# Optimization experiments

Hardware: AMD Instinct MI355X
Metric: run time of the kernel (lower is better)

## Reference

```python
import jax, jax.numpy as jnp
import numpy as np

N_NODES = 10000
N_EDGES = 160000
MUL0 = 128   # multiplicity of 0e in node input/output
MUL1 = 64    # multiplicity of 1o in node input/output
FC_IN = 8    # radial basis size (edge_scalar_attr dim)
FC_H = 64    # fc_neurons = [64, 64]
NUM_NEIGHBORS = 16.0
ANGLE = np.pi / 8.0
MID0 = MUL0 + MUL1   # 192 scalars in irreps_mid (simplified)
MID1 = MUL0 + MUL1   # 192 vectors (1o) in irreps_mid


def _inv_sqrt(d):
    return 1.0 / np.sqrt(d)


def setup_inputs() -> dict:
    key = jax.random.key(0)
    ks = jax.random.split(key, 18)
    rn = lambda k, shape: jax.random.normal(k, shape, dtype=jnp.float32)
    inp = {
        'node_input': rn(ks[0], (N_NODES, MUL0 + 3 * MUL1)),
        'edge_attr': rn(ks[1], (N_EDGES, 4)),            # 1x0e + 1x1o spherical harmonics
        'edge_scalar_attr': rn(ks[2], (N_EDGES, FC_IN)),
        # first Linear: node_input -> (node_features || node_self_out)
        'Wa0': rn(ks[3], (MUL0, MUL0)),   # 0e -> 0e (message branch)
        'Wa1': rn(ks[4], (MUL1, MUL1)),   # 1o -> 1o (message branch)
        'Wb0': rn(ks[5], (MUL0, MUL0)),   # 0e -> 0e (self branch)
        'Wb1': rn(ks[6], (MUL1, MUL1)),   # 1o -> 1o (self branch)
        # radial MLP
        'M1': rn(ks[7], (FC_IN, FC_H)),
        'M2': rn(ks[8], (FC_H, FC_H)),
        # per-instruction TP weight generators: [FC_H, mul] ('uvu', v=1 squeezed)
        'Wtp0': rn(ks[9], (FC_H, MUL0)),   # 0e x 0e -> 0e
        'Wtp1': rn(ks[10], (FC_H, MUL0)),  # 0e x 1o -> 1o
        'Wtp2': rn(ks[11], (FC_H, MUL1)),  # 1o x 0e -> 1o
        'Wtp3': rn(ks[12], (FC_H, MUL1)),  # 1o x 1o -> 0e
        # output Linear: irreps_mid (192x0e + 192x1o) -> 128x0e + 64x1o
        'Wo0': rn(ks[13], (MID0, MUL0)),
        'Wo1': rn(ks[14], (MID1, MUL1)),
        'edge_src': jax.random.randint(ks[15], (N_EDGES,), 0, N_NODES),
        'edge_dst': jax.random.randint(ks[16], (N_EDGES,), 0, N_NODES),
    }
    return inp


def _forward(node_input, edge_attr, edge_scalar_attr,
             Wa0, Wa1, Wb0, Wb1, M1, M2,
             Wtp0, Wtp1, Wtp2, Wtp3, Wo0, Wo1,
             edge_src, edge_dst):
    n = node_input.shape[0]
    x0 = node_input[:, :MUL0]                         # [N,128] 0e
    x1 = node_input[:, MUL0:].reshape(n, MUL1, 3)     # [N,64,3] 1o

    # Linear(node_input.irreps + irreps_node_output): split into message / self
    feat0 = (x0 @ Wa0) * _inv_sqrt(MUL0)
    feat1 = jnp.einsum('nvi,vu->nui', x1, Wa1) * _inv_sqrt(MUL1)
    self0 = (x0 @ Wb0) * _inv_sqrt(MUL0)
    self1 = jnp.einsum('nvi,vu->nui', x1, Wb1) * _inv_sqrt(MUL1)

    # gather node features to edges
    e0 = feat0[edge_src]                              # [E,128]
    e1 = feat1[edge_src]                              # [E,64,3]
    y0 = edge_attr[:, 0:1]                            # [E,1] 0e
    y1 = edge_attr[:, 1:4]                            # [E,3] 1o

    # radial MLP -> per-edge per-path 'uvu' weights (path param / sqrt(fc_out))
    h = jax.nn.gelu(edge_scalar_attr @ M1 * _inv_sqrt(FC_IN))
    h = jax.nn.gelu(h @ M2 * _inv_sqrt(FC_H))
    w0 = h @ Wtp0 * _inv_sqrt(FC_H)                   # [E,128]
    w1 = h @ Wtp1 * _inv_sqrt(FC_H)                   # [E,128]
    w2 = h @ Wtp2 * _inv_sqrt(FC_H)                   # [E,64]
    w3 = h @ Wtp3 * _inv_sqrt(FC_H)                   # [E,64]

    # CG tensor product paths (component normalization: alpha = sqrt(dim_out))
    mid0a = w0 * e0 * y0                                        # 0e x 0e -> 0e [E,128]
    mid0b = w3 * jnp.einsum('eui,ei->eu', e1, y1) * _inv_sqrt(3.0)  # 1o.1o -> 0e [E,64]
    mid1a = w1[:, :, None] * e0[:, :, None] * y1[:, None, :]   # 0e x 1o -> 1o [E,128,3]
    mid1b = w2[:, :, None] * e1 * y0[:, :, None]                # 1o x 0e -> 1o [E,64,3]

    e_cnt = edge_attr.shape[0]
    edge_mid = jnp.concatenate(
        [mid0a, mid0b, mid1a.reshape(e_cnt, -1), mid1b.reshape(e_cnt, -1)], axis=1)  # [E,768]

    # scatter-add to destination nodes, divide by sqrt(num_neighbors)
    agg = jax.ops.segment_sum(edge_mid, edge_dst, num_segments=n) * _inv_sqrt(NUM_NEIGHBORS)

    z0 = agg[:, :MID0]                                          # [N,192] 0e
    z1 = jnp.concatenate(
        [agg[:, MID0:MID0 + 3 * MUL0].reshape(n, MUL0, 3),
         agg[:, MID0 + 3 * MUL0:].reshape(n, MUL1, 3)], axis=1)  # [N,192,3] 1o

    conv0 = (z0 @ Wo0) * _inv_sqrt(MID0)
    conv1 = jnp.einsum('nvi,vu->nui', z1, Wo1) * _inv_sqrt(MID1)

    c = np.cos(ANGLE).astype(np.float32)
    s = np.sin(ANGLE).astype(np.float32)
    out0 = c * self0 + s * conv0                                 # [N,128]
    out1 = c * self1 + s * conv1                                 # [N,64,3]
    return jnp.concatenate([out0, out1.reshape(n, -1)], axis=1)  # [N,320]


def reference(node_input, edge_attr, edge_scalar_attr,
              Wa0, Wa1, Wb0, Wb1, M1, M2,
              Wtp0, Wtp1, Wtp2, Wtp3, Wo0, Wo1,
              edge_src, edge_dst):
    return _forward(node_input, edge_attr, edge_scalar_attr,
                    Wa0, Wa1, Wb0, Wb1, M1, M2,
                    Wtp0, Wtp1, Wtp2, Wtp3, Wo0, Wo1,
                    edge_src, edge_dst)
```

## Files before the change

### kernel.cpp

```cpp
#include <hip/hip_runtime.h>
#include <hip/hip_bf16.h>
#include <hip/hip_fp16.h>

#define N_NODES 10000
#define N_EDGES 160000
#define FEAT_W 320
#define CHUNK 32

typedef _Float16 half8 __attribute__((ext_vector_type(8)));
typedef float f32x4 __attribute__((ext_vector_type(4)));

__device__ __forceinline__ float gelu_tanh(float x) {
    float x3 = x * x * x;
    float y = 0.7978845608028654f * (x + 0.044715f * x3);
    float th = 1.f - 2.f / (__expf(2.f * y) + 1.f);
    return 0.5f * x * (1.f + th);
}

__global__ __launch_bounds__(320) void prep_kernel(
    const float* __restrict__ node_input,
    const float* __restrict__ Wa0, const float* __restrict__ Wa1,
    const float* __restrict__ Wb0, const float* __restrict__ Wb1,
    float* __restrict__ feat_tbl, float* __restrict__ self_tbl,
    const int* __restrict__ edge_dst, int* __restrict__ counts,
    int* __restrict__ rank,
    const float* __restrict__ Wtp0, const float* __restrict__ Wtp1,
    const float* __restrict__ Wtp2, const float* __restrict__ Wtp3,
    const float* __restrict__ Wo0,  const float* __restrict__ Wo1,
    __half* __restrict__ wtp_pack, __half* __restrict__ wo_pack)
{
    __shared__ __align__(16) float xT[FEAT_W][8];
    const int t = threadIdx.x;

    if (blockIdx.x < 1250) {
        const int node0 = blockIdx.x * 8;
        for (int q = t; q < 640; q += 320) {
            const int n = q / 80, c4 = q - n * 80;
            const float4 v = ((const float4*)(node_input + (size_t)(node0 + n) * FEAT_W))[c4];
            xT[c4 * 4 + 0][n] = v.x; xT[c4 * 4 + 1][n] = v.y;
            xT[c4 * 4 + 2][n] = v.z; xT[c4 * 4 + 3][n] = v.w;
        }
        __syncthreads();

        float accf[8] = {0,0,0,0,0,0,0,0}, accs[8] = {0,0,0,0,0,0,0,0};
        float scale;
        if (t < 128) {
            for (int v = 0; v < 128; ++v) {
                const float wa = Wa0[v * 128 + t];
                const float wb = Wb0[v * 128 + t];
                const float4 xa = *(const float4*)&xT[v][0];
                const float4 xb = *(const float4*)&xT[v][4];
                accf[0] += xa.x * wa; accf[1] += xa.y * wa; accf[2] += xa.z * wa; accf[3] += xa.w * wa;
                accf[4] += xb.x * wa; accf[5] += xb.y * wa; accf[6] += xb.z * wa; accf[7] += xb.w * wa;
                accs[0] += xa.x * wb; accs[1] += xa.y * wb; accs[2] += xa.z * wb; accs[3] += xa.w * wb;
                accs[4] += xb.x * wb; accs[5] += xb.y * wb; accs[6] += xb.z * wb; accs[7] += xb.w * wb;
            }
            scale = 0.08838834764831845f;
        } else {
            const int r = t - 128, u = r / 3, i = r - 3 * u;
            for (int v = 0; v < 64; ++v) {
                const float wa = Wa1[v * 64 + u];
                const float wb = Wb1[v * 64 + u];
                const int row = 128 + v * 3 + i;
                const float4 xa = *(const float4*)&xT[row][0];
                const float4 xb = *(const float4*)&xT[row][4];
                accf[0] += xa.x * wa; accf[1] += xa.y * wa; accf[2] += xa.z * wa; accf[3] += xa.w * wa;
                accf[4] += xb.x * wa; accf[5] += xb.y * wa; accf[6] += xb.z * wa; accf[7] += xb.w * wa;
                accs[0] += xa.x * wb; accs[1] += xa.y * wb; accs[2] += xa.z * wb; accs[3] += xa.w * wb;
                accs[4] += xb.x * wb; accs[5] += xb.y * wb; accs[6] += xb.z * wb; accs[7] += xb.w * wb;
            }
            scale = 0.125f;
        }
#pragma unroll
        for (int n = 0; n < 8; ++n) {
            feat_tbl[(size_t)(node0 + n) * FEAT_W + t] = accf[n] * scale;
            self_tbl[(size_t)(node0 + n) * FEAT_W + t] = accs[n] * scale;
        }
    } else if (blockIdx.x < 1750) {
        const int e = (blockIdx.x - 1250) * 320 + t;
        rank[e] = atomicAdd(&counts[edge_dst[e]], 1);
    } else {
        const int gid = (blockIdx.x - 1750) * 320 + t;
        if (gid < 1536) {
            const int lane = gid & 63;
            const int tile = gid >> 6;
            const int quad = lane >> 4, n16 = lane & 15;
            const int col = tile * 16 + n16;
            const float* src; int stride;
            if (col < 128)      { src = Wtp0 + col;         stride = 128; }
            else if (col < 256) { src = Wtp1 + (col - 128); stride = 128; }
            else if (col < 320) { src = Wtp2 + (col - 256); stride = 64;  }
            else                { src = Wtp3 + (col - 320); stride = 64;  }
            __half* dst = wtp_pack + (size_t)gid * 16;
#pragma unroll
            for (int s = 0; s < 2; ++s)
#pragma unroll
                for (int j = 0; j < 8; ++j)
                    dst[s * 8 + j] = (__half)src[(s * 32 + quad * 8 + j) * stride];
        } else if (gid < 38400) {
            const int i = gid - 1536;
            if (i < 24576) wo_pack[i] = (__half)Wo0[i];
            else           wo_pack[i] = (__half)Wo1[i - 24576];
        }
    }
}

__global__ __launch_bounds__(1024) void scan_kernel(
    const int* __restrict__ counts, int* __restrict__ offsets)
{
    __shared__ int wsum[16];
    const int wid = threadIdx.x >> 6, lane = threadIdx.x & 63;
    int base = 0;
    for (int c = 0; c < 10; ++c) {
        const int i = c * 1024 + threadIdx.x;
        const int v = (i < N_NODES) ? counts[i] : 0;
        int x = v;
#pragma unroll
        for (int off = 1; off < 64; off <<= 1) {
            int y = __shfl_up(x, off, 64);
            if (lane >= off) x += y;
        }
        if (lane == 63) wsum[wid] = x;
        __syncthreads();
        if (threadIdx.x < 16) {
            int s = wsum[threadIdx.x];
#pragma unroll
            for (int off = 1; off < 16; off <<= 1) {
                int y = __shfl_up(s, off, 64);
                if ((int)threadIdx.x >= off) s += y;
            }
            wsum[threadIdx.x] = s;
        }
        __syncthreads();
        const int waveoff = (wid == 0) ? 0 : wsum[wid - 1];
        const int excl = base + waveoff + x - v;
        if (i < N_NODES) offsets[i] = excl;
        const int tot = wsum[15];
        __syncthreads();
        base += tot;
    }
    if (threadIdx.x == 0) offsets[N_NODES] = base;
}

__global__ __launch_bounds__(512) void mlp_kernel(
    const float* __restrict__ esa,
    const float* __restrict__ M1,
    const float* __restrict__ M2,
    const int* __restrict__ edge_dst,
    const int* __restrict__ rank,
    const int* __restrict__ offsets,
    const int* __restrict__ edge_src,
    const float* __restrict__ edge_attr,
    __half* __restrict__ h2csr,
    int* __restrict__ srcs_csr,
    float* __restrict__ y4csr)
{
    __shared__ __align__(16) float sh[8][64];
    const int wave = threadIdx.x >> 6;
    const int lane = threadIdx.x & 63;
    const int e = blockIdx.x * 8 + wave;

    const int pos = offsets[edge_dst[e]] + rank[e];
    if (lane == 0) {
        srcs_csr[pos] = edge_src[e];
        ((float4*)y4csr)[pos] = ((const float4*)edge_attr)[e];
    }

    const float4 e0 = ((const float4*)(esa + (size_t)e * 8))[0];
    const float4 e1 = ((const float4*)(esa + (size_t)e * 8))[1];
    float h = e0.x * M1[0 * 64 + lane] + e0.y * M1[1 * 64 + lane]
            + e0.z * M1[2 * 64 + lane] + e0.w * M1[3 * 64 + lane]
            + e1.x * M1[4 * 64 + lane] + e1.y * M1[5 * 64 + lane]
            + e1.z * M1[6 * 64 + lane] + e1.w * M1[7 * 64 + lane];
    h = gelu_tanh(h * 0.35355339059327373f);
    sh[wave][lane] = h;
    __syncthreads();

    float h2 = 0.f;
    const float4* shp = (const float4*)sh[wave];
#pragma unroll
    for (int q = 0; q < 16; ++q) {
        const float4 s = shp[q];
        h2 += s.x * M2[(4 * q + 0) * 64 + lane];
        h2 += s.y * M2[(4 * q + 1) * 64 + lane];
        h2 += s.z * M2[(4 * q + 2) * 64 + lane];
        h2 += s.w * M2[(4 * q + 3) * 64 + lane];
    }
    h2 = gelu_tanh(h2 * 0.125f);
    h2csr[(size_t)pos * 64 + lane] = (__half)(h2 * 0.125f);
}

__global__ __launch_bounds__(384, 4) void gather_kernel(
    const int* __restrict__ offsets,
    const int* __restrict__ srcs_csr,
    const float* __restrict__ y4csr,
    const __half* __restrict__ h2csr,
    const __half* __restrict__ wtp_pack,
    const float* __restrict__ feat_tbl,
    const float* __restrict__ self_tbl,
    const __half* __restrict__ wo_pack,
    float* __restrict__ out)
{
    __shared__ __align__(16) __half wsh[CHUNK * 384];
    __shared__ __align__(16) char pool[CHUNK * 128];
    __shared__ float ys[CHUNK][4];
    __shared__ int   srcs[CHUNK];
    __half* h2s = (__half*)pool;
    float*  z   = (float*)pool;

    const int node = blockIdx.x;
    const int t = threadIdx.x;
    const int wave = t >> 6, lane = t & 63;
    const int quad = lane >> 4, n16 = lane & 15;
    const int G = t / 192;
    const int r = t - G * 192;

    const int beg = offsets[node], end = offsets[node + 1];

    int cb = beg;
    int ne = min(CHUNK, end - cb);
    half8 hreg = {};
    int   sreg = 0;
    float4 yreg = {0.f, 0.f, 0.f, 0.f};
    if (t < ne * 8) hreg = ((const half8*)(h2csr + (size_t)cb * 64))[t];
    if (t < ne)     { sreg = srcs_csr[cb + t]; yreg = ((const float4*)y4csr)[cb + t]; }

    half8 bf[4][2];
#pragma unroll
    for (int c = 0; c < 4; ++c) {
        const __half* p = wtp_pack + (size_t)((wave * 4 + c) * 64 + lane) * 16;
        bf[c][0] = *(const half8*)p;
        bf[c][1] = *(const half8*)(p + 8);
    }

    const int f0 = (r < 128) ? r : 128 + 3 * (r - 128);

    float acc = 0.f, acc3a = 0.f, acc3b = 0.f, acc3c = 0.f;

    for (;;) {
        if (t < ne) { srcs[t] = sreg; ((float4*)ys)[t] = yreg; }
        if (t < ne * 8) {
            const int eL = t >> 3, u = t & 7;
            *(half8*)((char*)h2s + eL * 128 + ((u * 16) ^ ((eL & 7) << 4))) = hreg;
        }
        __syncthreads();

#pragma unroll
        for (int g = 0; g < 2; ++g) {
            if (g * 16 < ne) {
                const int e = g * 16 + n16;
                const char* hb = (const char*)h2s + e * 128;
                const int sw = (e & 7) << 4;
                const half8 af0 = *(const half8*)(hb + ((quad * 16) ^ sw));
                const half8 af1 = *(const half8*)(hb + ((64 + quad * 16) ^ sw));
#pragma unroll
                for (int c = 0; c < 4; ++c) {
                    f32x4 acc4 = {0.f, 0.f, 0.f, 0.f};
                    acc4 = __builtin_amdgcn_mfma_f32_16x16x32_f16(af0, bf[c][0], acc4, 0, 0, 0);
                    acc4 = __builtin_amdgcn_mfma_f32_16x16x32_f16(af1, bf[c][1], acc4, 0, 0, 0);
                    const int colb = ((wave * 4 + c) * 16 + n16) * 2;
#pragma unroll
                    for (int rr = 0; rr < 4; ++rr) {
                        const int row = g * 16 + quad * 4 + rr;
                        *(__half*)((char*)wsh + row * 768 + (colb ^ (quad << 5))) =
                            (__half)acc4[rr];
                    }
                }
            }
        }

        const int cb2 = cb + CHUNK;
        const int ne2 = (cb2 < end) ? min(CHUNK, end - cb2) : 0;
        if (t < ne2 * 8) hreg = ((const half8*)(h2csr + (size_t)cb2 * 64))[t];
        if (t < ne2)     { sreg = srcs_csr[cb2 + t]; yreg = ((const float4*)y4csr)[cb2 + t]; }
        __syncthreads();

        const int h = (ne + 1) >> 1;
        const int eLo = G ? h : 0;
        const int eHi = G ? ne : h;
#define WRDC(ee, cc) __half2float(*(const __half*)((const char*)wsh + (ee) * 768 + (((cc) * 2) ^ ((((ee) >> 2) & 3) << 5))))
        if (r < 128) {
            int e = eLo;
            for (; e + 4 <= eHi; e += 4) {
                float wA[4], wB[4], v4[4]; int s4[4];
#pragma unroll
                for (int k = 0; k < 4; ++k) {
                    wA[k] = WRDC(e + k, r); wB[k] = WRDC(e + k, 128 + r);
                    s4[k] = srcs[e + k];
                }
#pragma unroll
                for (int k = 0; k < 4; ++k) v4[k] = feat_tbl[(size_t)s4[k] * FEAT_W + f0];
#pragma unroll
                for (int k = 0; k < 4; ++k) {
                    acc += wA[k] * v4[k] * ys[e + k][0];
                    const float p = wB[k] * v4[k];
                    acc3a += p * ys[e + k][1];
                    acc3b += p * ys[e + k][2];
                    acc3c += p * ys[e + k][3];
                }
            }
            for (; e < eHi; ++e) {
                const float v = feat_tbl[(size_t)srcs[e] * FEAT_W + f0];
                acc += WRDC(e, r) * v * ys[e][0];
                const float p = WRDC(e, 128 + r) * v;
                acc3a += p * ys[e][1]; acc3b += p * ys[e][2]; acc3c += p * ys[e][3];
            }
        } else {
            const int idx = r - 128;
            int e = eLo;
            for (; e + 4 <= eHi; e += 4) {
                float wC[4], wD[4], va[4], vb[4], vc[4]; int s4[4];
#pragma unroll
                for (int k = 0; k < 4; ++k) {
                    wC[k] = WRDC(e + k, 256 + idx); wD[k] = WRDC(e + k, 320 + idx);
                    s4[k] = srcs[e + k];
                }
#pragma unroll
                for (int k = 0; k < 4; ++k) {
                    const float* fr = feat_tbl + (size_t)s4[k] * FEAT_W;
                    va[k] = fr[f0]; vb[k] = fr[f0 + 1]; vc[k] = fr[f0 + 2];
                }
#pragma unroll
                for (int k = 0; k < 4; ++k) {
                    const float p = wC[k] * ys[e + k][0];
                    acc3a += p * va[k]; acc3b += p * vb[k]; acc3c += p * vc[k];
                    acc += wD[k] * (va[k] * ys[e + k][1] + vb[k] * ys[e + k][2]
                                  + vc[k] * ys[e + k][3]);
                }
            }
            for (; e < eHi; ++e) {
                const float* fr = feat_tbl + (size_t)srcs[e] * FEAT_W;
                const float va = fr[f0], vb = fr[f0 + 1], vc = fr[f0 + 2];
                const float p = WRDC(e, 256 + idx) * ys[e][0];
                acc3a += p * va; acc3b += p * vb; acc3c += p * vc;
                acc += WRDC(e, 320 + idx) * (va * ys[e][1] + vb * ys[e][2]
                                           + vc * ys[e][3]);
            }
        }
#undef WRDC

        if (!ne2) break;
        cb = cb2; ne = ne2;
        __syncthreads();
    }

    const float sZ = 0.25f;
    const float irt3 = 0.5773502691896258f;
    if (G == 0) {
        if (r < 128) {
            z[r]       = acc   * sZ;
            z[192 + r] = acc3a * sZ;
            z[384 + r] = acc3b * sZ;
            z[576 + r] = acc3c * sZ;
        } else {
            const int idx = r - 128;
            z[128 + idx] = acc * sZ * irt3;
            z[320 + idx] = acc3a * sZ;
            z[512 + idx] = acc3b * sZ;
            z[704 + idx] = acc3c * sZ;
        }
    }
    __syncthreads();
    if (G == 1) {
        if (r < 128) {
            z[r]       += acc   * sZ;
            z[192 + r] += acc3a * sZ;
            z[384 + r] += acc3b * sZ;
            z[576 + r] += acc3c * sZ;
        } else {
            const int idx = r - 128;
            z[128 + idx] += acc * sZ * irt3;
            z[320 + idx] += acc3a * sZ;
            z[512 + idx] += acc3b * sZ;
            z[704 + idx] += acc3c * sZ;
        }
    }
    __syncthreads();

    const float sA = 0.07216878364870323f;
    const float cR = 0.92387953251128674f;
    const float sR = 0.38268343236508978f;
    const __half* Wo0h = wo_pack;
    const __half* Wo1h = wo_pack + 24576;

    if (t < 128) {
        float conv = 0.f;
        const float4* z4 = (const float4*)z;
#pragma unroll 8
        for (int q = 0; q < 48; ++q) {
            const float4 zz = z4[q];
            conv += zz.x * (float)Wo0h[(4 * q + 0) * 128 + t];
            conv += zz.y * (float)Wo0h[(4 * q + 1) * 128 + t];
            conv += zz.z * (float)Wo0h[(4 * q + 2) * 128 + t];
            conv += zz.w * (float)Wo0h[(4 * q + 3) * 128 + t];
        }
        const float sv = self_tbl[(size_t)node * FEAT_W + t];
        out[(size_t)node * FEAT_W + t] = cR * sv + sR * conv * sA;
    } else if (t < 320) {
        const int idx = t - 128;
        const int i = idx >> 6, u = idx & 63;
        float conv = 0.f;
        const float4* z4 = (const float4*)(z + 192 + i * 192);
#pragma unroll 8
        for (int q = 0; q < 48; ++q) {
            const float4 zz = z4[q];
            conv += zz.x * (float)Wo1h[(4 * q + 0) * 64 + u];
            conv += zz.y * (float)Wo1h[(4 * q + 1) * 64 + u];
            conv += zz.z * (float)Wo1h[(4 * q + 2) * 64 + u];
            conv += zz.w * (float)Wo1h[(4 * q + 3) * 64 + u];
        }
        const int col = 128 + u * 3 + i;
        const float sv = self_tbl[(size_t)node * FEAT_W + col];
        out[(size_t)node * FEAT_W + col] = cR * sv + sR * conv * sA;
    }
}

extern "C" void kernel_launch(void* const* d_in, const int* in_sizes, int n_in,
                              void* d_out, int out_size, void* d_ws, size_t ws_size,
                              hipStream_t stream) {
    const float* node_input = (const float*)d_in[0];
    const float* edge_attr  = (const float*)d_in[1];
    const float* esa        = (const float*)d_in[2];
    const float* Wa0  = (const float*)d_in[3];
    const float* Wa1  = (const float*)d_in[4];
    const float* Wb0  = (const float*)d_in[5];
    const float* Wb1  = (const float*)d_in[6];
    const float* M1   = (const float*)d_in[7];
    const float* M2   = (const float*)d_in[8];
    const float* Wtp0 = (const float*)d_in[9];
    const float* Wtp1 = (const float*)d_in[10];
    const float* Wtp2 = (const float*)d_in[11];
    const float* Wtp3 = (const float*)d_in[12];
    const float* Wo0  = (const float*)d_in[13];
    const float* Wo1  = (const float*)d_in[14];
    const int* edge_src = (const int*)d_in[15];
    const int* edge_dst = (const int*)d_in[16];
    float* out = (float*)d_out;

    char* w = (char*)d_ws;
    float*  feat_tbl = (float*)w;           w += (size_t)N_NODES * FEAT_W * 4;
    float*  self_tbl = (float*)w;           w += (size_t)N_NODES * FEAT_W * 4;
    float*  y4csr    = (float*)w;           w += (size_t)N_EDGES * 4 * 4;
    __half* h2csr    = (__half*)w;          w += (size_t)N_EDGES * 64 * 2;
    __half* wtp_pack = (__half*)w;          w += (size_t)24576 * 2;
    __half* wo_pack  = (__half*)w;          w += (size_t)36864 * 2;
    int*    counts   = (int*)w;             w += (size_t)N_NODES * 4;
    int*    offsets  = (int*)w;             w += (size_t)(N_NODES + 1) * 4;
    int*    rank     = (int*)w;             w += (size_t)N_EDGES * 4;
    int*    srcs_csr = (int*)w;             w += (size_t)N_EDGES * 4;

    hipMemsetAsync(counts, 0, sizeof(int) * N_NODES, stream);

    prep_kernel<<<1870, 320, 0, stream>>>(node_input, Wa0, Wa1, Wb0, Wb1,
                                          feat_tbl, self_tbl,
                                          edge_dst, counts, rank,
                                          Wtp0, Wtp1, Wtp2, Wtp3, Wo0, Wo1,
                                          wtp_pack, wo_pack);
    scan_kernel<<<1, 1024, 0, stream>>>(counts, offsets);
    mlp_kernel<<<N_EDGES / 8, 512, 0, stream>>>(esa, M1, M2, edge_dst, rank, offsets,
                                                edge_src, edge_attr,
                                                h2csr, srcs_csr, y4csr);
    gather_kernel<<<N_NODES, 384, 0, stream>>>(offsets, srcs_csr, y4csr, h2csr,
                                               wtp_pack, feat_tbl, self_tbl,
                                               wo_pack, out);
}
```

Before: 408.7 us.

## Consume MFMA weight tiles directly in registers instead of staging through LDS

The per-edge tensor-product weights produced by MFMA are now used directly from the accumulator registers. Each wave multiplies them with gathered source features for its own column slice, accumulating per-lane partial sums that are reduced across quads with shuffles at the end. This removes the wsh LDS staging buffer, one barrier per chunk, and the two-group edge split. The cost is that each lane now issues more scattered feature gathers across its four edge rows and column groups, and the per-wave branch on irrep type may diverge.

```diff
diff --git a/kernel.cpp b/kernel.cpp
--- a/kernel.cpp
+++ b/kernel.cpp
@@ -201,7 +201,6 @@
     const __half* __restrict__ wo_pack,
     float* __restrict__ out)
 {
-    __shared__ __align__(16) __half wsh[CHUNK * 384];
     __shared__ __align__(16) char pool[CHUNK * 128];
     __shared__ float ys[CHUNK][4];
     __shared__ int   srcs[CHUNK];
@@ -212,8 +211,6 @@
     const int t = threadIdx.x;
     const int wave = t >> 6, lane = t & 63;
     const int quad = lane >> 4, n16 = lane & 15;
-    const int G = t / 192;
-    const int r = t - G * 192;
 
     const int beg = offsets[node], end = offsets[node + 1];
 
@@ -233,9 +230,7 @@
         bf[c][1] = *(const half8*)(p + 8);
     }
 
-    const int f0 = (r < 128) ? r : 128 + 3 * (r - 128);
-
-    float acc = 0.f, acc3a = 0.f, acc3b = 0.f, acc3c = 0.f;
+    float r0[4] = {0,0,0,0}, r1[4] = {0,0,0,0}, r2[4] = {0,0,0,0};
 
     for (;;) {
         if (t < ne) { srcs[t] = sreg; ((float4*)ys)[t] = yreg; }
@@ -245,134 +240,105 @@
         }
         __syncthreads();
 
-#pragma unroll
-        for (int g = 0; g < 2; ++g) {
-            if (g * 16 < ne) {
-                const int e = g * 16 + n16;
-                const char* hb = (const char*)h2s + e * 128;
-                const int sw = (e & 7) << 4;
-                const half8 af0 = *(const half8*)(hb + ((quad * 16) ^ sw));
-                const half8 af1 = *(const half8*)(hb + ((64 + quad * 16) ^ sw));
-#pragma unroll
-                for (int c = 0; c < 4; ++c) {
-                    f32x4 acc4 = {0.f, 0.f, 0.f, 0.f};
-                    acc4 = __builtin_amdgcn_mfma_f32_16x16x32_f16(af0, bf[c][0], acc4, 0, 0, 0);
-                    acc4 = __builtin_amdgcn_mfma_f32_16x16x32_f16(af1, bf[c][1], acc4, 0, 0, 0);
-                    const int colb = ((wave * 4 + c) * 16 + n16) * 2;
-#pragma unroll
-                    for (int rr = 0; rr < 4; ++rr) {
-                        const int row = g * 16 + quad * 4 + rr;
-                        *(__half*)((char*)wsh + row * 768 + (colb ^ (quad << 5))) =
-                            (__half)acc4[rr];
-                    }
-                }
-            }
-        }
-
         const int cb2 = cb + CHUNK;
         const int ne2 = (cb2 < end) ? min(CHUNK, end - cb2) : 0;
         if (t < ne2 * 8) hreg = ((const half8*)(h2csr + (size_t)cb2 * 64))[t];
         if (t < ne2)     { sreg = srcs_csr[cb2 + t]; yreg = ((const float4*)y4csr)[cb2 + t]; }
-        __syncthreads();
-
-        const int h = (ne + 1) >> 1;
-        const int eLo = G ? h : 0;
-        const int eHi = G ? ne : h;
-#define WRDC(ee, cc) __half2float(*(const __half*)((const char*)wsh + (ee) * 768 + (((cc) * 2) ^ ((((ee) >> 2) & 3) << 5))))
-        if (r < 128) {
-            int e = eLo;
-            for (; e + 4 <= eHi; e += 4) {
-                float wA[4], wB[4], v4[4]; int s4[4];
-#pragma unroll
-                for (int k = 0; k < 4; ++k) {
-                    wA[k] = WRDC(e + k, r); wB[k] = WRDC(e + k, 128 + r);
-                    s4[k] = srcs[e + k];
-                }
-#pragma unroll
-                for (int k = 0; k < 4; ++k) v4[k] = feat_tbl[(size_t)s4[k] * FEAT_W + f0];
-#pragma unroll
-                for (int k = 0; k < 4; ++k) {
-                    acc += wA[k] * v4[k] * ys[e + k][0];
-                    const float p = wB[k] * v4[k];
-                    acc3a += p * ys[e + k][1];
-                    acc3b += p * ys[e + k][2];
-                    acc3c += p * ys[e + k][3];
+
+#pragma unroll
+        for (int g = 0; g < 2; ++g) {
+            if (g * 16 < ne) {
+                const int er = g * 16 + n16;
+                const char* hb = (const char*)h2s + er * 128;
+                const int sw = (er & 7) << 4;
+                const half8 af0 = *(const half8*)(hb + ((quad * 16) ^ sw));
+                const half8 af1 = *(const half8*)(hb + ((64 + quad * 16) ^ sw));
+                f32x4 a0 = {0,0,0,0}, a1 = {0,0,0,0}, a2 = {0,0,0,0}, a3 = {0,0,0,0};
+                a0 = __builtin_amdgcn_mfma_f32_16x16x32_f16(af0, bf[0][0], a0, 0, 0, 0);
+                a0 = __builtin_amdgcn_mfma_f32_16x16x32_f16(af1, bf[0][1], a0, 0, 0, 0);
+                a1 = __builtin_amdgcn_mfma_f32_16x16x32_f16(af0, bf[1][0], a1, 0, 0, 0);
+                a1 = __builtin_amdgcn_mfma_f32_16x16x32_f16(af1, bf[1][1], a1, 0, 0, 0);
+                a2 = __builtin_amdgcn_mfma_f32_16x16x32_f16(af0, bf[2][0], a2, 0, 0, 0);
+                a2 = __builtin_amdgcn_mfma_f32_16x16x32_f16(af1, bf[2][1], a2, 0, 0, 0);
+                a3 = __builtin_amdgcn_mfma_f32_16x16x32_f16(af0, bf[3][0], a3, 0, 0, 0);
+                a3 = __builtin_amdgcn_mfma_f32_16x16x32_f16(af1, bf[3][1], a3, 0, 0, 0);
+
+#pragma unroll
+                for (int r = 0; r < 4; ++r) {
+                    const int e = g * 16 + quad * 4 + r;
+                    if (e < ne) {
+                        const float w4[4] = { a0[r], a1[r], a2[r], a3[r] };
+                        const float* fr = feat_tbl + (size_t)srcs[e] * FEAT_W;
+                        if (wave < 2) {
+                            const float y0 = ys[e][0];
+                            const int fb = wave * 64 + n16;
+#pragma unroll
+                            for (int c = 0; c < 4; ++c)
+                                r0[c] += w4[c] * fr[fb + c * 16] * y0;
+                        } else if (wave < 4) {
+                            const float y1 = ys[e][1], y2 = ys[e][2], y3 = ys[e][3];
+                            const int fb = (wave - 2) * 64 + n16;
+#pragma unroll
+                            for (int c = 0; c < 4; ++c) {
+                                const float p = w4[c] * fr[fb + c * 16];
+                                r0[c] += p * y1; r1[c] += p * y2; r2[c] += p * y3;
+                            }
+                        } else if (wave == 4) {
+                            const float y0 = ys[e][0];
+#pragma unroll
+                            for (int c = 0; c < 4; ++c) {
+                                const int f0 = 128 + 3 * (c * 16 + n16);
+                                const float p = w4[c] * y0;
+                                r0[c] += p * fr[f0];
+                                r1[c] += p * fr[f0 + 1];
+                                r2[c] += p * fr[f0 + 2];
+                            }
+                        } else {
+                            const float y1 = ys[e][1], y2 = ys[e][2], y3 = ys[e][3];
+#pragma unroll
+                            for (int c = 0; c < 4; ++c) {
+                                const int f0 = 128 + 3 * (c * 16 + n16);
+                                r0[c] += w4[c] * (fr[f0] * y1 + fr[f0 + 1] * y2
+                                                + fr[f0 + 2] * y3);
+                            }
+                        }
+                    }
                 }
             }
-            for (; e < eHi; ++e) {
-                const float v = feat_tbl[(size_t)srcs[e] * FEAT_W + f0];
-                acc += WRDC(e, r) * v * ys[e][0];
-                const float p = WRDC(e, 128 + r) * v;
-                acc3a += p * ys[e][1]; acc3b += p * ys[e][2]; acc3c += p * ys[e][3];
-            }
-        } else {
-            const int idx = r - 128;
-            int e = eLo;
-            for (; e + 4 <= eHi; e += 4) {
-                float wC[4], wD[4], va[4], vb[4], vc[4]; int s4[4];
-#pragma unroll
-                for (int k = 0; k < 4; ++k) {
-                    wC[k] = WRDC(e + k, 256 + idx); wD[k] = WRDC(e + k, 320 + idx);
-                    s4[k] = srcs[e + k];
-                }
-#pragma unroll
-                for (int k = 0; k < 4; ++k) {
-                    const float* fr = feat_tbl + (size_t)s4[k] * FEAT_W;
-                    va[k] = fr[f0]; vb[k] = fr[f0 + 1]; vc[k] = fr[f0 + 2];
-                }
-#pragma unroll
-                for (int k = 0; k < 4; ++k) {
-                    const float p = wC[k] * ys[e + k][0];
-                    acc3a += p * va[k]; acc3b += p * vb[k]; acc3c += p * vc[k];
-                    acc += wD[k] * (va[k] * ys[e + k][1] + vb[k] * ys[e + k][2]
-                                  + vc[k] * ys[e + k][3]);
-                }
-            }
-            for (; e < eHi; ++e) {
-                const float* fr = feat_tbl + (size_t)srcs[e] * FEAT_W;
-                const float va = fr[f0], vb = fr[f0 + 1], vc = fr[f0 + 2];
-                const float p = WRDC(e, 256 + idx) * ys[e][0];
-                acc3a += p * va; acc3b += p * vb; acc3c += p * vc;
-                acc += WRDC(e, 320 + idx) * (va * ys[e][1] + vb * ys[e][2]
-                                           + vc * ys[e][3]);
-            }
-        }
-#undef WRDC
+        }
 
         if (!ne2) break;
         cb = cb2; ne = ne2;
         __syncthreads();
     }
-
+    __syncthreads();
+
+#pragma unroll
+    for (int c = 0; c < 4; ++c) {
+        r0[c] += __shfl_xor(r0[c], 16, 64); r0[c] += __shfl_xor(r0[c], 32, 64);
+        r1[c] += __shfl_xor(r1[c], 16, 64); r1[c] += __shfl_xor(r1[c], 32, 64);
+        r2[c] += __shfl_xor(r2[c], 16, 64); r2[c] += __shfl_xor(r2[c], 32, 64);
+    }
     const float sZ = 0.25f;
     const float irt3 = 0.5773502691896258f;
-    if (G == 0) {
-        if (r < 128) {
-            z[r]       = acc   * sZ;
-            z[192 + r] = acc3a * sZ;
-            z[384 + r] = acc3b * sZ;
-            z[576 + r] = acc3c * sZ;
-        } else {
-            const int idx = r - 128;
-            z[128 + idx] = acc * sZ * irt3;
-            z[320 + idx] = acc3a * sZ;
-            z[512 + idx] = acc3b * sZ;
-            z[704 + idx] = acc3c * sZ;
-        }
-    }
-    __syncthreads();
-    if (G == 1) {
-        if (r < 128) {
-            z[r]       += acc   * sZ;
-            z[192 + r] += acc3a * sZ;
-            z[384 + r] += acc3b * sZ;
-            z[576 + r] += acc3c * sZ;
-        } else {
-            const int idx = r - 128;
-            z[128 + idx] += acc * sZ * irt3;
-            z[320 + idx] += acc3a * sZ;
-            z[512 + idx] += acc3b * sZ;
-            z[704 + idx] += acc3c * sZ;
+    if (lane < 16) {
+#pragma unroll
+        for (int c = 0; c < 4; ++c) {
+            const int cn = c * 16 + n16;
+            if (wave < 2) {
+                z[wave * 64 + cn] = r0[c] * sZ;
+            } else if (wave < 4) {
+                const int cB = (wave - 2) * 64 + cn;
+                z[192 + cB] = r0[c] * sZ;
+                z[384 + cB] = r1[c] * sZ;
+                z[576 + cB] = r2[c] * sZ;
+            } else if (wave == 4) {
+                z[320 + cn] = r0[c] * sZ;
+                z[512 + cn] = r1[c] * sZ;
+                z[704 + cn] = r2[c] * sZ;
+            } else {
+                z[128 + cn] = r0[c] * sZ * irt3;
+            }
         }
     }
     __syncthreads();
```

New measurement: 443.0 us. 1.08x slower.
